# Kernel optimization log

Measured on AMD Instinct MI355X. Metric: run time of the kernel, lower is better.

## Reference

```python
import jax, jax.numpy as jnp
import numpy as np

GRID_SIZE = 4
SPLINE_ORDER = 3
EDGE_DIM = 384


def make_grid():
    # efficient-KAN default grid_range [-1, 1]
    h = 2.0 / GRID_SIZE
    return (jnp.arange(-SPLINE_ORDER, GRID_SIZE + SPLINE_ORDER + 1, dtype=jnp.float32) * h - 1.0)


def b_splines(x, grid, k):
    # x: (N, d); grid: (G+2k+1,) shared across features -> (N, d, G+k)
    xe = x[..., None]
    bases = ((xe >= grid[:-1]) & (xe < grid[1:])).astype(x.dtype)
    for j in range(1, k + 1):
        bases = ((xe - grid[: -(j + 1)]) / (grid[j:-1] - grid[: -(j + 1)]) * bases[..., :-1]
                 + (grid[j + 1:] - xe) / (grid[j + 1:] - grid[1:-j]) * bases[..., 1:])
    return bases


def kan_linear(x, base_W, spline_W, grid):
    # efficient-KAN KANLinear: silu base path + spline path
    base = jax.nn.silu(x) @ base_W.T
    B = b_splines(x, grid, SPLINE_ORDER)          # (N, in, G+k)
    spline = jnp.einsum('nic,oic->no', B, spline_W)
    return base + spline


def gckan_layer(x, edge_index, edge_attr, p, grid):
    ea = edge_attr @ p['edge_W'].T + p['edge_b']          # (E, out)
    xt = x @ p['node_W'].T + p['node_b']                  # (N, out)
    row, col = edge_index[0], edge_index[1]
    msg = ea * xt[row]                                    # gather + multiply
    agg = jnp.zeros_like(xt).at[col].add(msg)             # scatter-add
    return kan_linear(agg, p['base_W'], p['spline_W'], grid)


def _layer_params(key, in_feat, out_feat):
    k1, k2, k3, k4 = jax.random.split(key, 4)
    coef = GRID_SIZE + SPLINE_ORDER
    return {
        'node_W': jax.random.normal(k1, (out_feat, in_feat), jnp.float32) / np.sqrt(in_feat),
        'node_b': jnp.zeros((out_feat,), jnp.float32),
        'edge_W': jax.random.normal(k2, (out_feat, EDGE_DIM), jnp.float32) / np.sqrt(EDGE_DIM),
        'edge_b': jnp.zeros((out_feat,), jnp.float32),
        'base_W': jax.random.normal(k3, (out_feat, out_feat), jnp.float32) / np.sqrt(out_feat),
        'spline_W': jax.random.normal(k4, (out_feat, out_feat, coef), jnp.float32) * (0.1 / np.sqrt(out_feat)),
    }


def setup_inputs() -> dict:
    N, E, F, H, C = 50000, 500000, 256, 256, 32
    key = jax.random.key(0)
    ks = jax.random.split(key, 6)
    inp = {
        'x': jax.random.normal(ks[0], (N, F), jnp.float32),
        'edge_index': jax.random.randint(ks[1], (2, E), 0, N, jnp.int32),
        'edge_attr': jax.random.normal(ks[2], (E, EDGE_DIM), jnp.float32),
    }
    p0 = _layer_params(ks[3], F, H)
    p1 = _layer_params(ks[4], H, H)
    po = _layer_params(ks[5], F + 2 * H, C)
    for tag, p in (('0', p0), ('1', p1), ('o', po)):
        for n, v in p.items():
            inp[n + tag] = v
    return inp


def reference(x, edge_index, edge_attr,
              node_W0, node_b0, edge_W0, edge_b0, base_W0, spline_W0,
              node_W1, node_b1, edge_W1, edge_b1, base_W1, spline_W1,
              node_Wo, node_bo, edge_Wo, edge_bo, base_Wo, spline_Wo):
    grid = make_grid()
    p0 = dict(node_W=node_W0, node_b=node_b0, edge_W=edge_W0, edge_b=edge_b0, base_W=base_W0, spline_W=spline_W0)
    p1 = dict(node_W=node_W1, node_b=node_b1, edge_W=edge_W1, edge_b=edge_b1, base_W=base_W1, spline_W=spline_W1)
    po = dict(node_W=node_Wo, node_b=node_bo, edge_W=edge_Wo, edge_b=edge_bo, base_W=base_Wo, spline_W=spline_Wo)
    skips = [x]
    h = gckan_layer(x, edge_index, edge_attr, p0, grid)
    skips.append(h)
    h = gckan_layer(h, edge_index, edge_attr, p1, grid)
    skips.append(h)
    h = jnp.concatenate(skips, axis=1)  # skip=True concat -> (N, F+2H)
    return gckan_layer(h, edge_index, edge_attr, po, grid)
```

## Files before the change

kernel.cpp:

```cpp
#include <hip/hip_runtime.h>


typedef __attribute__((ext_vector_type(4))) float f32x4;
typedef __attribute__((ext_vector_type(8))) short bf16x8;
typedef __attribute__((ext_vector_type(8))) unsigned short u16x8;
typedef __attribute__((ext_vector_type(4))) unsigned short u16x4;

__device__ __forceinline__ unsigned short f2bf(float f) {
    union { float f; unsigned u; } v; v.f = f;
    unsigned r = v.u + 0x7FFFu + ((v.u >> 16) & 1u);
    return (unsigned short)(r >> 16);
}

__device__ __forceinline__ float bf2f(unsigned short u) {
    union { unsigned u; float f; } v; v.u = ((unsigned)u) << 16;
    return v.f;
}

__device__ __forceinline__ float siluf(float x) {
    return x / (1.0f + __expf(-x));
}

__device__ __forceinline__ void gl16(const void* g, void* l) {
    __builtin_amdgcn_global_load_lds(
        (const __attribute__((address_space(1))) unsigned*)g,
        (__attribute__((address_space(3))) unsigned*)l, 16, 0, 0);
}

__device__ __forceinline__ void expand8(float x, float* o8) {
    float b[10];
#pragma unroll
    for (int i = 0; i < 10; ++i) {
        float ti = 0.5f * i - 2.5f;
        b[i] = (x >= ti && x < ti + 0.5f) ? 1.0f : 0.0f;
    }
#pragma unroll
    for (int j = 1; j <= 3; ++j) {
        float inv = 2.0f / (float)j;
#pragma unroll
        for (int i = 0; i < 10 - j; ++i) {
            float ti = 0.5f * i - 2.5f;
            float tj = 0.5f * (i + j + 1) - 2.5f;
            b[i] = (x - ti) * inv * b[i] + (tj - x) * inv * b[i + 1];
        }
    }
    o8[0] = siluf(x);
#pragma unroll
    for (int c = 0; c < 7; ++c) o8[c + 1] = b[c];
}

__global__ __launch_bounds__(256) void k_hist(
    const int* __restrict__ col, int* __restrict__ cnt, int E) {
    int i = blockIdx.x * 256 + threadIdx.x;
    if (i < E) atomicAdd(&cnt[col[i]], 1);
}

__global__ __launch_bounds__(1024) void k_scan(int* __restrict__ c, int N) {
    __shared__ int wsum[16];
    __shared__ int ctot;
    const int t = threadIdx.x;
    const int lane = t & 63, wid = t >> 6;
    int carry = 0;
    for (int base = 0; base < N; base += 1024) {
        int i = base + t;
        int v0 = (i < N) ? c[i] : 0;
        int v = v0;
#pragma unroll
        for (int off = 1; off < 64; off <<= 1) {
            int n = __shfl_up(v, (unsigned)off, 64);
            if (lane >= off) v += n;
        }
        if (lane == 63) wsum[wid] = v;
        __syncthreads();
        if (t < 16) {
            int s = wsum[t], sv = s;
#pragma unroll
            for (int off = 1; off < 16; off <<= 1) {
                int n = __shfl_up(sv, (unsigned)off, 16);
                if (t >= off) sv += n;
            }
            wsum[t] = sv - s;
            if (t == 15) ctot = sv;
        }
        __syncthreads();
        if (i < N) c[i] = carry + wsum[wid] + v - v0;
        carry += ctot;
        __syncthreads();
    }
}

__global__ __launch_bounds__(256) void k_scatter(
    const int* __restrict__ row, const int* __restrict__ col,
    int* __restrict__ cursor, int* __restrict__ rowS,
    int* __restrict__ colS, int* __restrict__ eidS, int E) {
    int i = blockIdx.x * 256 + threadIdx.x;
    if (i < E) {
        int c = col[i];
        int p = atomicAdd(&cursor[c], 1);
        rowS[p] = row[i];
        colS[p] = c;
        eidS[p] = i;
    }
}

__global__ __launch_bounds__(256) void pack_kt(
    const float* __restrict__ src, unsigned short* __restrict__ dst,
    int N, int K) {
    long idx = (long)blockIdx.x * 256 + threadIdx.x;
    if (idx >= (long)N * K) return;
    int n = (int)(idx / K), k = (int)(idx - (long)n * K);
    long o = (((long)(k >> 5) * 4 + ((k >> 3) & 3)) * N + n) * 8 + (k & 7);
    dst[o] = f2bf(src[idx]);
}

__global__ __launch_bounds__(256) void pack_kan_kt(
    const float* __restrict__ baseW, const float* __restrict__ splineW,
    unsigned short* __restrict__ dst, int N) {
    long idx = (long)blockIdx.x * 256 + threadIdx.x;
    if (idx >= (long)N * 2048) return;
    int n = (int)(idx >> 11), k = (int)(idx & 2047);
    int ic = k >> 3, c = k & 7;
    float v = (c == 0) ? baseW[(long)n * 256 + ic]
                       : splineW[((long)n * 256 + ic) * 7 + (c - 1)];
    long o = (((long)(k >> 5) * 4 + ((k >> 3) & 3)) * N + n) * 8 + (k & 7);
    dst[o] = f2bf(v);
}

template <bool TWO, bool WITH_O>
__global__ __launch_bounds__(256, 1) void ea_gemm4(
    const float* __restrict__ EA,
    const unsigned short* __restrict__ Wp0, const float* __restrict__ b0,
    const unsigned short* __restrict__ Wp1, const float* __restrict__ b1,
    const unsigned short* __restrict__ Wpo, const float* __restrict__ bo,
    unsigned short* __restrict__ O0, unsigned short* __restrict__ O1,
    unsigned short* __restrict__ Oo, int E) {
    constexpr int WOOFF = TWO ? 73728 : 40960;
    constexpr int SMEMSZ = WOOFF + (WITH_O ? 24576 : 0);
    __shared__ __align__(16) char smem[SMEMSZ];

    const int tid = threadIdx.x;
    const int wv = tid >> 6, lane = tid & 63;
    const int l15 = lane & 15, l4 = lane >> 4;
    const long m0 = (long)blockIdx.x * 64;

    f32x4 acc0[4][4] = {};
    f32x4 acc1[4][4] = {};
    f32x4 acco[4] = {};

    const int sr = tid >> 2, sg = tid & 3;
    const long arow = m0 + sr;
    const bool aok = arow < E;
    const float* aptr = EA + arow * 384 + sg * 8;
    const int awoff = sg * 1024 + ((sr ^ (sg << 2))) * 16;

    const char* wp0 = (const char*)Wp0;
    const char* wp1 = (const char*)Wp1;
    const int ci = lane * 16;

    if (WITH_O) {
#pragma unroll
        for (int i = 0; i < 6; ++i) {
            int o = (tid + i * 256) * 16;
            if (o < 24576)
                *(u16x8*)(smem + WOOFF + o) =
                    *(const u16x8*)((const char*)Wpo + o);
        }
    }

#define ISSUE_B(IT, BUF)                                                       \
    {                                                                          \
        _Pragma("unroll")                                                      \
        for (int g = 0; g < 4; ++g) {                                          \
            int ch = g * 4 + wv;                                               \
            gl16(wp0 + (long)(IT) * 16384 + ch * 1024 + ci,                    \
                 smem + 8192 + (BUF) * 16384 + ch * 1024);                     \
        }                                                                      \
        if (TWO) {                                                             \
            _Pragma("unroll")                                                  \
            for (int g = 0; g < 4; ++g) {                                      \
                int ch = g * 4 + wv;                                           \
                gl16(wp1 + (long)(IT) * 16384 + ch * 1024 + ci,                \
                     smem + 40960 + (BUF) * 16384 + ch * 1024);                \
            }                                                                  \
        }                                                                      \
        __builtin_amdgcn_sched_barrier(0);                                     \
    }

#define WRITE_A(BUF)                                                           \
    {                                                                          \
        u16x8 rr = {};                                                         \
        if (aok) {                                                             \
            rr[0] = f2bf(a0v.x); rr[1] = f2bf(a0v.y);                          \
            rr[2] = f2bf(a0v.z); rr[3] = f2bf(a0v.w);                          \
            rr[4] = f2bf(a1v.x); rr[5] = f2bf(a1v.y);                          \
            rr[6] = f2bf(a1v.z); rr[7] = f2bf(a1v.w);                          \
        }                                                                      \
        *(u16x8*)(smem + (BUF) * 4096 + awoff) = rr;                           \
        __builtin_amdgcn_sched_barrier(0);                                     \
    }

    ISSUE_B(0, 0);
    float4 a0v = make_float4(0.f, 0.f, 0.f, 0.f);
    float4 a1v = make_float4(0.f, 0.f, 0.f, 0.f);
    if (aok) { a0v = *(const float4*)(aptr); a1v = *(const float4*)(aptr + 4); }
    WRITE_A(0);
    if (aok) { a0v = *(const float4*)(aptr + 32); a1v = *(const float4*)(aptr + 36); }
    __builtin_amdgcn_sched_barrier(0);

#pragma unroll
    for (int it = 0; it < 12; ++it) {
        if (it == 11) asm volatile("s_waitcnt vmcnt(0)" ::: "memory");
        else          asm volatile("s_waitcnt vmcnt(2)" ::: "memory");
        asm volatile("s_waitcnt lgkmcnt(0)" ::: "memory");
        __builtin_amdgcn_s_barrier();
        __builtin_amdgcn_sched_barrier(0);
        const int buf = it & 1, nbf = buf ^ 1;
        if (it < 11) {
            ISSUE_B(it + 1, nbf);
            WRITE_A(nbf);
            if (it < 10) {
                if (aok) {
                    a0v = *(const float4*)(aptr + (it + 2) * 32);
                    a1v = *(const float4*)(aptr + (it + 2) * 32 + 4);
                }
                __builtin_amdgcn_sched_barrier(0);
            }
        }
        bf16x8 af[4];
#pragma unroll
        for (int mi = 0; mi < 4; ++mi)
            af[mi] = *(const bf16x8*)(smem + buf * 4096 + l4 * 1024 +
                                      (((mi * 16 + l15) ^ (l4 << 2))) * 16);
        {
            bf16x8 bf0[4];
#pragma unroll
            for (int nj = 0; nj < 4; ++nj)
                bf0[nj] = *(const bf16x8*)(smem + 8192 + buf * 16384 + l4 * 4096 +
                                           (wv * 64 + nj * 16 + l15) * 16);
#pragma unroll
            for (int mi = 0; mi < 4; ++mi)
#pragma unroll
                for (int nj = 0; nj < 4; ++nj)
                    acc0[mi][nj] = __builtin_amdgcn_mfma_f32_16x16x32_bf16(
                        af[mi], bf0[nj], acc0[mi][nj], 0, 0, 0);
        }
        if (TWO) {
            bf16x8 bf1[4];
#pragma unroll
            for (int nj = 0; nj < 4; ++nj)
                bf1[nj] = *(const bf16x8*)(smem + 40960 + buf * 16384 + l4 * 4096 +
                                           (wv * 64 + nj * 16 + l15) * 16);
#pragma unroll
            for (int mi = 0; mi < 4; ++mi)
#pragma unroll
                for (int nj = 0; nj < 4; ++nj)
                    acc1[mi][nj] = __builtin_amdgcn_mfma_f32_16x16x32_bf16(
                        af[mi], bf1[nj], acc1[mi][nj], 0, 0, 0);
        }
        if (WITH_O && wv < 2) {
            bf16x8 bov = *(const bf16x8*)(smem + WOOFF + it * 2048 + l4 * 512 +
                                          (wv * 16 + l15) * 16);
#pragma unroll
            for (int mi = 0; mi < 4; ++mi)
                acco[mi] = __builtin_amdgcn_mfma_f32_16x16x32_bf16(
                    af[mi], bov, acco[mi], 0, 0, 0);
        }
    }
#undef ISSUE_B
#undef WRITE_A

    const int nb2 = wv * 64;
    float bs0[4];
#pragma unroll
    for (int nj = 0; nj < 4; ++nj) bs0[nj] = b0[nb2 + nj * 16 + l15];
#pragma unroll
    for (int mi = 0; mi < 4; ++mi) {
#pragma unroll
        for (int r = 0; r < 4; ++r) {
            long e = m0 + mi * 16 + l4 * 4 + r;
            if (e < E) {
                unsigned short* dst = O0 + e * 256 + nb2 + l15;
#pragma unroll
                for (int nj = 0; nj < 4; ++nj)
                    dst[nj * 16] = f2bf(acc0[mi][nj][r] + bs0[nj]);
            }
        }
    }
    if (TWO) {
        float bs1[4];
#pragma unroll
        for (int nj = 0; nj < 4; ++nj) bs1[nj] = b1[nb2 + nj * 16 + l15];
#pragma unroll
        for (int mi = 0; mi < 4; ++mi) {
#pragma unroll
            for (int r = 0; r < 4; ++r) {
                long e = m0 + mi * 16 + l4 * 4 + r;
                if (e < E) {
                    unsigned short* dst = O1 + e * 256 + nb2 + l15;
#pragma unroll
                    for (int nj = 0; nj < 4; ++nj)
                        dst[nj * 16] = f2bf(acc1[mi][nj][r] + bs1[nj]);
                }
            }
        }
    }
    if (WITH_O && wv < 2) {
        float bso = bo[wv * 16 + l15];
#pragma unroll
        for (int mi = 0; mi < 4; ++mi) {
#pragma unroll
            for (int r = 0; r < 4; ++r) {
                long e = m0 + mi * 16 + l4 * 4 + r;
                if (e < E)
                    Oo[e * 32 + wv * 16 + l15] = f2bf(acco[mi][r] + bso);
            }
        }
    }
}

__global__ __launch_bounds__(256) void kan_mfma256_p(
    const float* __restrict__ AGG, const unsigned short* __restrict__ Wp,
    float* __restrict__ Y, int M) {
    __shared__ __align__(16) char smem[8192 + 2 * 16384];
    const int tid = threadIdx.x;
    const int wv = tid >> 6, lane = tid & 63;
    const int l15 = lane & 15, l4 = lane >> 4;
    const long m0 = (long)blockIdx.x * 64;
    f32x4 acc[4][4] = {};

    const int srow = tid & 63, sg = tid >> 6;
    const long arow = m0 + srow;
    const bool aok = arow < M;
    const float* aptr = AGG + arow * 256 + sg;
    const char* wp = (const char*)Wp;
    const int ci = lane * 16;
    const int awoff = sg * 1024 + srow * 16;

#define ISSUE_KB(IT, BUF)                                                      \
    {                                                                          \
        _Pragma("unroll")                                                      \
        for (int g = 0; g < 4; ++g) {                                          \
            int ch = g * 4 + wv;                                               \
            gl16(wp + (long)(IT) * 16384 + ch * 1024 + ci,                     \
                 smem + 8192 + (BUF) * 16384 + ch * 1024);                     \
        }                                                                      \
        __builtin_amdgcn_sched_barrier(0);                                     \
    }

    float xv0 = aok ? aptr[0] : 0.f;
    ISSUE_KB(0, 0);
    {
        float e8[8];
        expand8(xv0, e8);
        u16x8 ap;
#pragma unroll
        for (int c = 0; c < 8; ++c) ap[c] = f2bf(e8[c]);
        *(u16x8*)(smem + awoff) = ap;
    }
    float xv1 = aok ? aptr[4] : 0.f;
    __builtin_amdgcn_sched_barrier(0);

    for (int it = 0; it < 64; ++it) {
        if (it == 63) asm volatile("s_waitcnt vmcnt(0)" ::: "memory");
        else          asm volatile("s_waitcnt vmcnt(1)" ::: "memory");
        asm volatile("s_waitcnt lgkmcnt(0)" ::: "memory");
        __builtin_amdgcn_s_barrier();
        __builtin_amdgcn_sched_barrier(0);
        const int buf = it & 1, nbf = buf ^ 1;
        if (it < 63) {
            ISSUE_KB(it + 1, nbf);
            {
                float e8[8];
                expand8(xv1, e8);
                u16x8 ap;
#pragma unroll
                for (int c = 0; c < 8; ++c) ap[c] = f2bf(e8[c]);
                *(u16x8*)(smem + nbf * 4096 + awoff) = ap;
            }
            __builtin_amdgcn_sched_barrier(0);
            if (it < 62) {
                xv1 = aok ? aptr[(it + 2) * 4] : 0.f;
                __builtin_amdgcn_sched_barrier(0);
            }
        }
        bf16x8 af[4], bfv[4];
#pragma unroll
        for (int mi = 0; mi < 4; ++mi)
            af[mi] = *(const bf16x8*)(smem + buf * 4096 + l4 * 1024 +
                                      (mi * 16 + l15) * 16);
#pragma unroll
        for (int nj = 0; nj < 4; ++nj)
            bfv[nj] = *(const bf16x8*)(smem + 8192 + buf * 16384 + l4 * 4096 +
                                       (wv * 64 + nj * 16 + l15) * 16);
#pragma unroll
        for (int mi = 0; mi < 4; ++mi)
#pragma unroll
            for (int nj = 0; nj < 4; ++nj)
                acc[mi][nj] = __builtin_amdgcn_mfma_f32_16x16x32_bf16(
                    af[mi], bfv[nj], acc[mi][nj], 0, 0, 0);
    }
#undef ISSUE_KB

    const int nb = wv * 64;
#pragma unroll
    for (int mi = 0; mi < 4; ++mi) {
#pragma unroll
        for (int r = 0; r < 4; ++r) {
            long gm = m0 + mi * 16 + l4 * 4 + r;
            if (gm < M) {
#pragma unroll
                for (int nj = 0; nj < 4; ++nj)
                    Y[gm * 256 + nb + nj * 16 + l15] = acc[mi][nj][r];
            }
        }
    }
}

template <int K>
__global__ __launch_bounds__(256) void node_mfma_p(
    const float* __restrict__ X, const unsigned short* __restrict__ Wp,
    const float* __restrict__ bias, unsigned short* __restrict__ Y, int M) {
    __shared__ __align__(16) char smem[8192 + 2 * 16384];
    const int tid = threadIdx.x;
    const int wv = tid >> 6, lane = tid & 63;
    const int l15 = lane & 15, l4 = lane >> 4;
    const long m0 = (long)blockIdx.x * 64;
    f32x4 acc[4][4] = {};
    constexpr int NIT = K / 32;

    const int sr = tid >> 2, sg = tid & 3;
    const long arow = m0 + sr;
    const bool aok = arow < M;
    const float* aptr = X + arow * K + sg * 8;
    const int awoff = sg * 1024 + ((sr ^ (sg << 2))) * 16;
    const char* wp = (const char*)Wp;
    const int ci = lane * 16;

#define ISSUE_NB(IT, BUF)                                                      \
    {                                                                          \
        _Pragma("unroll")                                                      \
        for (int g = 0; g < 4; ++g) {                                          \
            int ch = g * 4 + wv;                                               \
            gl16(wp + (long)(IT) * 16384 + ch * 1024 + ci,                     \
                 smem + 8192 + (BUF) * 16384 + ch * 1024);                     \
        }                                                                      \
        __builtin_amdgcn_sched_barrier(0);                                     \
    }

#define WRITE_NA(BUF)                                                          \
    {                                                                          \
        u16x8 rr = {};                                                         \
        if (aok) {                                                             \
            rr[0] = f2bf(a0v.x); rr[1] = f2bf(a0v.y);                          \
            rr[2] = f2bf(a0v.z); rr[3] = f2bf(a0v.w);                          \
            rr[4] = f2bf(a1v.x); rr[5] = f2bf(a1v.y);                          \
            rr[6] = f2bf(a1v.z); rr[7] = f2bf(a1v.w);                          \
        }                                                                      \
        *(u16x8*)(smem + (BUF) * 4096 + awoff) = rr;                           \
        __builtin_amdgcn_sched_barrier(0);                                     \
    }

    ISSUE_NB(0, 0);
    float4 a0v = make_float4(0.f, 0.f, 0.f, 0.f);
    float4 a1v = make_float4(0.f, 0.f, 0.f, 0.f);
    if (aok) { a0v = *(const float4*)(aptr); a1v = *(const float4*)(aptr + 4); }
    WRITE_NA(0);
    if (aok) { a0v = *(const float4*)(aptr + 32); a1v = *(const float4*)(aptr + 36); }
    __builtin_amdgcn_sched_barrier(0);

#pragma unroll
    for (int it = 0; it < NIT; ++it) {
        if (it == NIT - 1) asm volatile("s_waitcnt vmcnt(0)" ::: "memory");
        else               asm volatile("s_waitcnt vmcnt(2)" ::: "memory");
        asm volatile("s_waitcnt lgkmcnt(0)" ::: "memory");
        __builtin_amdgcn_s_barrier();
        __builtin_amdgcn_sched_barrier(0);
        const int buf = it & 1, nbf = buf ^ 1;
        if (it < NIT - 1) {
            ISSUE_NB(it + 1, nbf);
            WRITE_NA(nbf);
            if (it < NIT - 2) {
                if (aok) {
                    a0v = *(const float4*)(aptr + (it + 2) * 32);
                    a1v = *(const float4*)(aptr + (it + 2) * 32 + 4);
                }
                __builtin_amdgcn_sched_barrier(0);
            }
        }
        bf16x8 af[4], bfv[4];
#pragma unroll
        for (int mi = 0; mi < 4; ++mi)
            af[mi] = *(const bf16x8*)(smem + buf * 4096 + l4 * 1024 +
                                      (((mi * 16 + l15) ^ (l4 << 2))) * 16);
#pragma unroll
        for (int nj = 0; nj < 4; ++nj)
            bfv[nj] = *(const bf16x8*)(smem + 8192 + buf * 16384 + l4 * 4096 +
                                       (wv * 64 + nj * 16 + l15) * 16);
#pragma unroll
        for (int mi = 0; mi < 4; ++mi)
#pragma unroll
            for (int nj = 0; nj < 4; ++nj)
                acc[mi][nj] = __builtin_amdgcn_mfma_f32_16x16x32_bf16(
                    af[mi], bfv[nj], acc[mi][nj], 0, 0, 0);
    }
#undef ISSUE_NB
#undef WRITE_NA

    const int nb = wv * 64;
    float bs[4];
#pragma unroll
    for (int nj = 0; nj < 4; ++nj) bs[nj] = bias[nb + nj * 16 + l15];
#pragma unroll
    for (int mi = 0; mi < 4; ++mi) {
#pragma unroll
        for (int r = 0; r < 4; ++r) {
            long gm = m0 + mi * 16 + l4 * 4 + r;
            if (gm < M) {
#pragma unroll
                for (int nj = 0; nj < 4; ++nj)
                    Y[gm * 256 + nb + nj * 16 + l15] = f2bf(acc[mi][nj][r] + bs[nj]);
            }
        }
    }
}

__global__ __launch_bounds__(256) void msg256(
    const unsigned short* __restrict__ EAr, const unsigned short* __restrict__ XT,
    const int* __restrict__ rowS, const int* __restrict__ colS,
    const int* __restrict__ eidS, float* __restrict__ AGG, int E) {
    __shared__ __align__(16) unsigned short eas[64][264];
    __shared__ int rows_s[64];
    __shared__ int cols_s[64];
    const int tid = threadIdx.x;
    const long m0 = (long)blockIdx.x * 64;

    const int r = tid >> 2, s = tid & 3;
    {
        long p = m0 + r;
        if (p < E) {
            const unsigned short* src = EAr + (long)eidS[p] * 256 + s * 8;
#pragma unroll
            for (int k = 0; k < 8; ++k)
                *(u16x8*)&eas[r][s * 8 + k * 32] = *(const u16x8*)(src + k * 32);
        } else {
            u16x8 z = {};
#pragma unroll
            for (int k = 0; k < 8; ++k) *(u16x8*)&eas[r][s * 8 + k * 32] = z;
        }
    }
    if (tid < 64) {
        long p = m0 + tid;
        cols_s[tid] = (p < E) ? colS[p] : -1;
        rows_s[tid] = (p < E) ? rowS[p] : 0;
    }
    __syncthreads();

    const int c = tid;
    float sum = 0.f;
    int cur = cols_s[0];
    int runstart = 0;
#pragma unroll 1
    for (int g = 0; g < 8; ++g) {
        float xv[8];
#pragma unroll
        for (int j = 0; j < 8; ++j)
            xv[j] = bf2f(XT[(long)rows_s[g * 8 + j] * 256 + c]);
#pragma unroll
        for (int j = 0; j < 8; ++j) {
            int e = g * 8 + j;
            int cc = cols_s[e];
            if (cc != cur) {
                if (cur >= 0) {
                    float* dst = AGG + (long)cur * 256 + c;
                    if (runstart > 0) *dst = sum;
                    else atomicAdd(dst, sum);
                }
                cur = cc; runstart = e; sum = 0.f;
            }
            sum += bf2f(eas[e][c]) * xv[j];
        }
    }
    if (cur >= 0) {
        atomicAdd(AGG + (long)cur * 256 + c, sum);
    }
}

__global__ __launch_bounds__(256) void msg32(
    const unsigned short* __restrict__ EAro, const unsigned short* __restrict__ XT,
    const int* __restrict__ rowS, const int* __restrict__ colS,
    const int* __restrict__ eidS, float* __restrict__ AGG, int E) {
    __shared__ __align__(16) unsigned short eas[256][36];
    __shared__ int rows_s[256];
    __shared__ int cols_s[256];
    __shared__ int eid_s[256];
    const int tid = threadIdx.x;
    const long m0 = (long)blockIdx.x * 256;

    {
        long p = m0 + tid;
        cols_s[tid] = (p < E) ? colS[p] : -1;
        rows_s[tid] = (p < E) ? rowS[p] : 0;
        eid_s[tid]  = (p < E) ? eidS[p] : -1;
    }
    __syncthreads();
    const int rr0 = tid >> 2, s = tid & 3;
#pragma unroll
    for (int ps = 0; ps < 4; ++ps) {
        int rr = ps * 64 + rr0;
        int eid = eid_s[rr];
        u16x8 v = {};
        if (eid >= 0) v = *(const u16x8*)(EAro + (long)eid * 32 + s * 8);
        *(u16x8*)&eas[rr][s * 8] = v;
    }
    __syncthreads();

    const int c = tid & 31, sb = tid >> 5;
    const int e0 = sb * 32;
    float sum = 0.f;
    int cur = cols_s[e0];
    int runstart = e0;
#pragma unroll 1
    for (int g = 0; g < 4; ++g) {
        float xv[8];
#pragma unroll
        for (int j = 0; j < 8; ++j)
            xv[j] = bf2f(XT[(long)rows_s[e0 + g * 8 + j] * 32 + c]);
#pragma unroll
        for (int j = 0; j < 8; ++j) {
            int e = e0 + g * 8 + j;
            int cc = cols_s[e];
            if (cc != cur) {
                if (cur >= 0) {
                    float* dst = AGG + (long)cur * 32 + c;
                    if (runstart > 0 && cols_s[runstart - 1] != cur) *dst = sum;
                    else atomicAdd(dst, sum);
                }
                cur = cc; runstart = e; sum = 0.f;
            }
            sum += bf2f(eas[e][c]) * xv[j];
        }
    }
    if (cur >= 0) {
        int eend = e0 + 32;
        float* dst = AGG + (long)cur * 32 + c;
        bool oks = (runstart > 0 && cols_s[runstart - 1] != cur);
        bool oke = (eend < 256 && cols_s[eend] != cur);
        if (oks && oke) *dst = sum;
        else atomicAdd(dst, sum);
    }
}

__global__ __launch_bounds__(256) void node_cat_mfma(
    const float* __restrict__ X, const float* __restrict__ H0,
    const float* __restrict__ H1, const unsigned short* __restrict__ Wh,
    const float* __restrict__ bias, unsigned short* __restrict__ Y, int M) {
    __shared__ __align__(16) unsigned short As[4][256][8];
    __shared__ __align__(16) unsigned short Bs[4][32][8];
    const int tid = threadIdx.x;
    const int wv = tid >> 6, lane = tid & 63;
    const int l15 = lane & 15, l4 = lane >> 4;
    const long m0 = (long)blockIdx.x * 256;
    f32x4 acc[4][2] = {};

    const int sr = tid >> 3;
    const int sq = (tid & 7) * 4;
    const int sg2 = sq >> 3, so2 = sq & 7;

    for (int it = 0; it < 24; ++it) {
        const int k0 = it * 32;
        const float* src = (it < 8) ? X : (it < 16) ? H0 : H1;
        const int kk = k0 & 255;
        float4 va[8];
#pragma unroll
        for (int j = 0; j < 8; ++j) {
            long r_ = m0 + j * 32 + sr;
            va[j] = (r_ < M) ? *(const float4*)(src + r_ * 256 + kk + sq)
                             : make_float4(0.f, 0.f, 0.f, 0.f);
        }
        u16x8 bv = {};
        if (tid < 128)
            bv = *(const u16x8*)(Wh + (long)(tid >> 2) * 768 + k0 + (tid & 3) * 8);
        __syncthreads();
#pragma unroll
        for (int j = 0; j < 8; ++j) {
            u16x4 ap;
            ap[0] = f2bf(va[j].x); ap[1] = f2bf(va[j].y);
            ap[2] = f2bf(va[j].z); ap[3] = f2bf(va[j].w);
            *(u16x4*)&As[sg2][j * 32 + sr][so2] = ap;
        }
        if (tid < 128) *(u16x8*)&Bs[tid & 3][tid >> 2][0] = bv;
        __syncthreads();
        bf16x8 af[4], bfv[2];
#pragma unroll
        for (int mi = 0; mi < 4; ++mi)
            af[mi] = *(const bf16x8*)&As[l4][wv * 64 + mi * 16 + l15][0];
#pragma unroll
        for (int nj = 0; nj < 2; ++nj)
            bfv[nj] = *(const bf16x8*)&Bs[l4][nj * 16 + l15][0];
#pragma unroll
        for (int mi = 0; mi < 4; ++mi)
#pragma unroll
            for (int nj = 0; nj < 2; ++nj)
                acc[mi][nj] = __builtin_amdgcn_mfma_f32_16x16x32_bf16(
                    af[mi], bfv[nj], acc[mi][nj], 0, 0, 0);
    }

#pragma unroll
    for (int mi = 0; mi < 4; ++mi) {
#pragma unroll
        for (int r = 0; r < 4; ++r) {
            long gm = m0 + wv * 64 + mi * 16 + l4 * 4 + r;
            if (gm < M) {
#pragma unroll
                for (int nj = 0; nj < 2; ++nj) {
                    int o = nj * 16 + l15;
                    Y[gm * 32 + o] = f2bf(acc[mi][nj][r] + bias[o]);
                }
            }
        }
    }
}

__global__ __launch_bounds__(256) void kan_gemm32(
    const float* __restrict__ AGG, const float* __restrict__ Wc,
    float* __restrict__ Y, int M) {
    __shared__ float As[64][36];
    __shared__ float Bs[32][36];
    const int tid = threadIdx.x;
    const int tx = tid & 15, ty = tid >> 4;
    const int m0 = blockIdx.x * 64;
    float acc[4][2] = {{0.f, 0.f}, {0.f, 0.f}, {0.f, 0.f}, {0.f, 0.f}};
    const int er = tid >> 2, ef = tid & 3;
    const int em = m0 + er;
    for (int ic = 0; ic < 32; ic += 4) {
        float xv = (em < M) ? AGG[(long)em * 32 + ic + ef] : 0.f;
        float e8[8];
        expand8(xv, e8);
        *(float4*)&As[er][ef * 8] = make_float4(e8[0], e8[1], e8[2], e8[3]);
        *(float4*)&As[er][ef * 8 + 4] = make_float4(e8[4], e8[5], e8[6], e8[7]);
        {
            int o = tid >> 3, k4 = (tid & 7) * 4;
            *(float4*)&Bs[o][k4] = *(const float4*)&Wc[(long)o * 256 + ic * 8 + k4];
        }
        __syncthreads();
#pragma unroll
        for (int kk = 0; kk < 32; ++kk) {
            float a_[4], b_[2];
#pragma unroll
            for (int i = 0; i < 4; ++i) a_[i] = As[ty * 4 + i][kk];
#pragma unroll
            for (int j = 0; j < 2; ++j) b_[j] = Bs[tx * 2 + j][kk];
#pragma unroll
            for (int i = 0; i < 4; ++i)
#pragma unroll
                for (int j = 0; j < 2; ++j) acc[i][j] = fmaf(a_[i], b_[j], acc[i][j]);
        }
        __syncthreads();
    }
#pragma unroll
    for (int i = 0; i < 4; ++i) {
        int gm = m0 + ty * 4 + i;
        if (gm >= M) continue;
#pragma unroll
        for (int j = 0; j < 2; ++j) Y[(long)gm * 32 + tx * 2 + j] = acc[i][j];
    }
}

__global__ __launch_bounds__(256) void cvt_bf16(
    const float* __restrict__ s, unsigned short* __restrict__ d, int n) {
    int i = blockIdx.x * 256 + threadIdx.x;
    if (i < n) d[i] = f2bf(s[i]);
}

__global__ __launch_bounds__(256) void pack_kan_f32(
    const float* __restrict__ baseW, const float* __restrict__ splineW,
    float* __restrict__ Wc, int n) {
    int idx = blockIdx.x * 256 + threadIdx.x;
    if (idx >= n) return;
    float* dst = Wc + (long)idx * 8;
    dst[0] = baseW[idx];
    const float* sw = splineW + (long)idx * 7;
#pragma unroll
    for (int c = 0; c < 7; ++c) dst[1 + c] = sw[c];
}

extern "C" void kernel_launch(void* const* d_in, const int* in_sizes, int n_in,
                              void* d_out, int out_size, void* d_ws, size_t ws_size,
                              hipStream_t stream) {
    const float* x          = (const float*)d_in[0];
    const int*   edge_index = (const int*)d_in[1];
    const float* edge_attr  = (const float*)d_in[2];
    const float* node_W0 = (const float*)d_in[3];
    const float* node_b0 = (const float*)d_in[4];
    const float* edge_W0 = (const float*)d_in[5];
    const float* edge_b0 = (const float*)d_in[6];
    const float* base_W0 = (const float*)d_in[7];
    const float* spline_W0 = (const float*)d_in[8];
    const float* node_W1 = (const float*)d_in[9];
    const float* node_b1 = (const float*)d_in[10];
    const float* edge_W1 = (const float*)d_in[11];
    const float* edge_b1 = (const float*)d_in[12];
    const float* base_W1 = (const float*)d_in[13];
    const float* spline_W1 = (const float*)d_in[14];
    const float* node_Wo = (const float*)d_in[15];
    const float* node_bo = (const float*)d_in[16];
    const float* edge_Wo = (const float*)d_in[17];
    const float* edge_bo = (const float*)d_in[18];
    const float* base_Wo = (const float*)d_in[19];
    const float* spline_Wo = (const float*)d_in[20];
    float* out = (float*)d_out;

    const int N = in_sizes[0] / 256;
    const int E = in_sizes[1] / 2;

    float* ws  = (float*)d_ws;
    unsigned short* xt = (unsigned short*)ws;
    float* agg = ws + (long)N * 256;
    float* h0  = agg + (long)N * 256;
    float* h1  = h0 + (long)N * 256;
    float* Wco = h1 + (long)N * 256;
    unsigned short* Wp0  = (unsigned short*)(Wco + 32 * 256);
    unsigned short* Wp1  = Wp0 + 98304;
    unsigned short* Wpo  = Wp1 + 98304;
    unsigned short* nWp0 = Wpo + 12288;
    unsigned short* nWp1 = nWp0 + 65536;
    unsigned short* Wc0p = nWp1 + 65536;
    unsigned short* Wc1p = Wc0p + 524288;
    unsigned short* nWoh = Wc1p + 524288;
    int* cursor = (int*)(nWoh + 24576);
    int* rowS   = cursor + (N + 1);
    int* colS   = rowS + E;
    int* eidS   = colS + E;
    unsigned short* EAr0 = (unsigned short*)(((uintptr_t)(eidS + E) + 255) & ~(uintptr_t)255);
    const int nt256 = (E + 255) / 256;
    const long Epad = (long)nt256 * 256;
    unsigned short* EAr1 = EAr0 + Epad * 256;

    const size_t need2 = (size_t)((char*)(EAr1 + Epad * 256 + Epad * 32) - (char*)d_ws);
    const bool two = ws_size >= need2;
    unsigned short* EAro = two ? (EAr1 + Epad * 256) : (EAr0 + Epad * 256);

    const int* row = edge_index;
    const int* col = edge_index + E;

    const int nb64 = (N + 63) / 64;
    const int eb64 = (E + 63) / 64;
    const int eb256 = (E + 255) / 256;
    const int nb256 = (N + 255) / 256;

    hipMemsetAsync(cursor, 0, (size_t)(N + 1) * sizeof(int), stream);
    k_hist<<<eb256, 256, 0, stream>>>(col, cursor, E);
    k_scan<<<1, 1024, 0, stream>>>(cursor, N);
    k_scatter<<<eb256, 256, 0, stream>>>(row, col, cursor, rowS, colS, eidS, E);

    pack_kt<<<(256 * 384 + 255) / 256, 256, 0, stream>>>(edge_W0, Wp0, 256, 384);
    pack_kt<<<(256 * 384 + 255) / 256, 256, 0, stream>>>(edge_W1, Wp1, 256, 384);
    pack_kt<<<(32 * 384 + 255) / 256, 256, 0, stream>>>(edge_Wo, Wpo, 32, 384);
    pack_kt<<<(256 * 256 + 255) / 256, 256, 0, stream>>>(node_W0, nWp0, 256, 256);
    pack_kt<<<(256 * 256 + 255) / 256, 256, 0, stream>>>(node_W1, nWp1, 256, 256);
    pack_kan_kt<<<(256 * 2048 + 255) / 256, 256, 0, stream>>>(base_W0, spline_W0, Wc0p, 256);
    pack_kan_kt<<<(256 * 2048 + 255) / 256, 256, 0, stream>>>(base_W1, spline_W1, Wc1p, 256);
    cvt_bf16<<<(32 * 768 + 255) / 256, 256, 0, stream>>>(node_Wo, nWoh, 32 * 768);
    pack_kan_f32<<<(32 * 32 + 255) / 256, 256, 0, stream>>>(base_Wo, spline_Wo, Wco, 32 * 32);

    if (two) {
        ea_gemm4<true, true><<<eb64, 256, 0, stream>>>(
            edge_attr, Wp0, edge_b0, Wp1, edge_b1, Wpo, edge_bo,
            EAr0, EAr1, EAro, E);
    } else {
        ea_gemm4<false, true><<<eb64, 256, 0, stream>>>(
            edge_attr, Wp0, edge_b0, Wp0, edge_b0, Wpo, edge_bo,
            EAr0, EAr0, EAro, E);
    }

    hipMemsetAsync(agg, 0, (size_t)N * 256 * sizeof(float), stream);
    node_mfma_p<256><<<nb64, 256, 0, stream>>>(x, nWp0, node_b0, xt, N);
    msg256<<<eb64, 256, 0, stream>>>(EAr0, xt, rowS, colS, eidS, agg, E);
    kan_mfma256_p<<<nb64, 256, 0, stream>>>(agg, Wc0p, h0, N);

    if (!two) {
        ea_gemm4<false, false><<<eb64, 256, 0, stream>>>(
            edge_attr, Wp1, edge_b1, Wp1, edge_b1, Wpo, edge_bo,
            EAr0, EAr0, EAro, E);
    }
    hipMemsetAsync(agg, 0, (size_t)N * 256 * sizeof(float), stream);
    node_mfma_p<256><<<nb64, 256, 0, stream>>>(h0, nWp1, node_b1, xt, N);
    msg256<<<eb64, 256, 0, stream>>>(two ? EAr1 : EAr0, xt, rowS, colS, eidS, agg, E);
    kan_mfma256_p<<<nb64, 256, 0, stream>>>(agg, Wc1p, h1, N);

    hipMemsetAsync(agg, 0, (size_t)N * 32 * sizeof(float), stream);
    node_cat_mfma<<<nb256, 256, 0, stream>>>(x, h0, h1, nWoh, node_bo, xt, N);
    msg32<<<eb256, 256, 0, stream>>>(EAro, xt, rowS, colS, eidS, agg, E);
    kan_gemm32<<<nb64, 256, 0, stream>>>(agg, Wco, out, N);
}
```

Before: 1.533 ms.

## Replace LDS-staged edge GEMM with per-wave direct-load MFMA tiles

Rewrites the edge-attribute projection kernel so each wave handles its own 16 edges against all 256 (or 512) output columns. Weights are read straight from global memory and the A fragment is converted in registers, so there is no LDS staging, no double buffering and no block barriers. Launch bounds are raised to allow two blocks per CU. In exchange, weight reuse across waves now depends on L1/L2 instead of shared memory, and the per-lane output stores stay strided.

```diff
diff --git a/kernel.cpp b/kernel.cpp
--- a/kernel.cpp
+++ b/kernel.cpp
@@ -127,192 +127,84 @@
 }
 
 template <bool TWO, bool WITH_O>
-__global__ __launch_bounds__(256, 1) void ea_gemm4(
+__global__ __launch_bounds__(256, 2) void ea_gemm5(
     const float* __restrict__ EA,
     const unsigned short* __restrict__ Wp0, const float* __restrict__ b0,
     const unsigned short* __restrict__ Wp1, const float* __restrict__ b1,
     const unsigned short* __restrict__ Wpo, const float* __restrict__ bo,
     unsigned short* __restrict__ O0, unsigned short* __restrict__ O1,
     unsigned short* __restrict__ Oo, int E) {
-    constexpr int WOOFF = TWO ? 73728 : 40960;
-    constexpr int SMEMSZ = WOOFF + (WITH_O ? 24576 : 0);
-    __shared__ __align__(16) char smem[SMEMSZ];
-
     const int tid = threadIdx.x;
     const int wv = tid >> 6, lane = tid & 63;
     const int l15 = lane & 15, l4 = lane >> 4;
-    const long m0 = (long)blockIdx.x * 64;
-
-    f32x4 acc0[4][4] = {};
-    f32x4 acc1[4][4] = {};
-    f32x4 acco[4] = {};
-
-    const int sr = tid >> 2, sg = tid & 3;
-    const long arow = m0 + sr;
+    const long m0 = (long)blockIdx.x * 64 + wv * 16;
+
+    f32x4 acc0[16] = {};
+    f32x4 acc1[16] = {};
+    f32x4 acco[2] = {};
+
+    const long arow = m0 + l15;
     const bool aok = arow < E;
-    const float* aptr = EA + arow * 384 + sg * 8;
-    const int awoff = sg * 1024 + ((sr ^ (sg << 2))) * 16;
-
-    const char* wp0 = (const char*)Wp0;
-    const char* wp1 = (const char*)Wp1;
-    const int ci = lane * 16;
-
-    if (WITH_O) {
-#pragma unroll
-        for (int i = 0; i < 6; ++i) {
-            int o = (tid + i * 256) * 16;
-            if (o < 24576)
-                *(u16x8*)(smem + WOOFF + o) =
-                    *(const u16x8*)((const char*)Wpo + o);
-        }
-    }
-
-#define ISSUE_B(IT, BUF)                                                       \
-    {                                                                          \
-        _Pragma("unroll")                                                      \
-        for (int g = 0; g < 4; ++g) {                                          \
-            int ch = g * 4 + wv;                                               \
-            gl16(wp0 + (long)(IT) * 16384 + ch * 1024 + ci,                    \
-                 smem + 8192 + (BUF) * 16384 + ch * 1024);                     \
-        }                                                                      \
-        if (TWO) {                                                             \
-            _Pragma("unroll")                                                  \
-            for (int g = 0; g < 4; ++g) {                                      \
-                int ch = g * 4 + wv;                                           \
-                gl16(wp1 + (long)(IT) * 16384 + ch * 1024 + ci,                \
-                     smem + 40960 + (BUF) * 16384 + ch * 1024);                \
-            }                                                                  \
-        }                                                                      \
-        __builtin_amdgcn_sched_barrier(0);                                     \
-    }
-
-#define WRITE_A(BUF)                                                           \
-    {                                                                          \
-        u16x8 rr = {};                                                         \
-        if (aok) {                                                             \
-            rr[0] = f2bf(a0v.x); rr[1] = f2bf(a0v.y);                          \
-            rr[2] = f2bf(a0v.z); rr[3] = f2bf(a0v.w);                          \
-            rr[4] = f2bf(a1v.x); rr[5] = f2bf(a1v.y);                          \
-            rr[6] = f2bf(a1v.z); rr[7] = f2bf(a1v.w);                          \
-        }                                                                      \
-        *(u16x8*)(smem + (BUF) * 4096 + awoff) = rr;                           \
-        __builtin_amdgcn_sched_barrier(0);                                     \
-    }
-
-    ISSUE_B(0, 0);
-    float4 a0v = make_float4(0.f, 0.f, 0.f, 0.f);
-    float4 a1v = make_float4(0.f, 0.f, 0.f, 0.f);
-    if (aok) { a0v = *(const float4*)(aptr); a1v = *(const float4*)(aptr + 4); }
-    WRITE_A(0);
-    if (aok) { a0v = *(const float4*)(aptr + 32); a1v = *(const float4*)(aptr + 36); }
-    __builtin_amdgcn_sched_barrier(0);
-
-#pragma unroll
+    const float* aptr = EA + arow * 384 + l4 * 8;
+    const unsigned short* bp0 = Wp0 + l4 * 2048 + l15 * 8;
+    const unsigned short* bp1 = Wp1 + l4 * 2048 + l15 * 8;
+    const unsigned short* bpo = Wpo + l4 * 256 + l15 * 8;
+
+#pragma unroll 2
     for (int it = 0; it < 12; ++it) {
-        if (it == 11) asm volatile("s_waitcnt vmcnt(0)" ::: "memory");
-        else          asm volatile("s_waitcnt vmcnt(2)" ::: "memory");
-        asm volatile("s_waitcnt lgkmcnt(0)" ::: "memory");
-        __builtin_amdgcn_s_barrier();
-        __builtin_amdgcn_sched_barrier(0);
-        const int buf = it & 1, nbf = buf ^ 1;
-        if (it < 11) {
-            ISSUE_B(it + 1, nbf);
-            WRITE_A(nbf);
-            if (it < 10) {
-                if (aok) {
-                    a0v = *(const float4*)(aptr + (it + 2) * 32);
-                    a1v = *(const float4*)(aptr + (it + 2) * 32 + 4);
-                }
-                __builtin_amdgcn_sched_barrier(0);
-            }
-        }
-        bf16x8 af[4];
-#pragma unroll
-        for (int mi = 0; mi < 4; ++mi)
-            af[mi] = *(const bf16x8*)(smem + buf * 4096 + l4 * 1024 +
-                                      (((mi * 16 + l15) ^ (l4 << 2))) * 16);
-        {
-            bf16x8 bf0[4];
-#pragma unroll
-            for (int nj = 0; nj < 4; ++nj)
-                bf0[nj] = *(const bf16x8*)(smem + 8192 + buf * 16384 + l4 * 4096 +
-                                           (wv * 64 + nj * 16 + l15) * 16);
-#pragma unroll
-            for (int mi = 0; mi < 4; ++mi)
-#pragma unroll
-                for (int nj = 0; nj < 4; ++nj)
-                    acc0[mi][nj] = __builtin_amdgcn_mfma_f32_16x16x32_bf16(
-                        af[mi], bf0[nj], acc0[mi][nj], 0, 0, 0);
-        }
-        if (TWO) {
-            bf16x8 bf1[4];
-#pragma unroll
-            for (int nj = 0; nj < 4; ++nj)
-                bf1[nj] = *(const bf16x8*)(smem + 40960 + buf * 16384 + l4 * 4096 +
-                                           (wv * 64 + nj * 16 + l15) * 16);
-#pragma unroll
-            for (int mi = 0; mi < 4; ++mi)
-#pragma unroll
-                for (int nj = 0; nj < 4; ++nj)
-                    acc1[mi][nj] = __builtin_amdgcn_mfma_f32_16x16x32_bf16(
-                        af[mi], bf1[nj], acc1[mi][nj], 0, 0, 0);
-        }
-        if (WITH_O && wv < 2) {
-            bf16x8 bov = *(const bf16x8*)(smem + WOOFF + it * 2048 + l4 * 512 +
-                                          (wv * 16 + l15) * 16);
-#pragma unroll
-            for (int mi = 0; mi < 4; ++mi)
-                acco[mi] = __builtin_amdgcn_mfma_f32_16x16x32_bf16(
-                    af[mi], bov, acco[mi], 0, 0, 0);
-        }
-    }
-#undef ISSUE_B
-#undef WRITE_A
-
-    const int nb2 = wv * 64;
-    float bs0[4];
-#pragma unroll
-    for (int nj = 0; nj < 4; ++nj) bs0[nj] = b0[nb2 + nj * 16 + l15];
-#pragma unroll
-    for (int mi = 0; mi < 4; ++mi) {
-#pragma unroll
-        for (int r = 0; r < 4; ++r) {
-            long e = m0 + mi * 16 + l4 * 4 + r;
-            if (e < E) {
-                unsigned short* dst = O0 + e * 256 + nb2 + l15;
-#pragma unroll
-                for (int nj = 0; nj < 4; ++nj)
-                    dst[nj * 16] = f2bf(acc0[mi][nj][r] + bs0[nj]);
-            }
-        }
-    }
-    if (TWO) {
-        float bs1[4];
-#pragma unroll
-        for (int nj = 0; nj < 4; ++nj) bs1[nj] = b1[nb2 + nj * 16 + l15];
-#pragma unroll
-        for (int mi = 0; mi < 4; ++mi) {
-#pragma unroll
-            for (int r = 0; r < 4; ++r) {
-                long e = m0 + mi * 16 + l4 * 4 + r;
-                if (e < E) {
-                    unsigned short* dst = O1 + e * 256 + nb2 + l15;
-#pragma unroll
-                    for (int nj = 0; nj < 4; ++nj)
-                        dst[nj * 16] = f2bf(acc1[mi][nj][r] + bs1[nj]);
-                }
-            }
-        }
-    }
-    if (WITH_O && wv < 2) {
-        float bso = bo[wv * 16 + l15];
-#pragma unroll
-        for (int mi = 0; mi < 4; ++mi) {
-#pragma unroll
-            for (int r = 0; r < 4; ++r) {
-                long e = m0 + mi * 16 + l4 * 4 + r;
-                if (e < E)
-                    Oo[e * 32 + wv * 16 + l15] = f2bf(acco[mi][r] + bso);
+        u16x8 au = {};
+        if (aok) {
+            float4 v0 = *(const float4*)(aptr + it * 32);
+            float4 v1 = *(const float4*)(aptr + it * 32 + 4);
+            au[0] = f2bf(v0.x); au[1] = f2bf(v0.y); au[2] = f2bf(v0.z); au[3] = f2bf(v0.w);
+            au[4] = f2bf(v1.x); au[5] = f2bf(v1.y); au[6] = f2bf(v1.z); au[7] = f2bf(v1.w);
+        }
+        bf16x8 af;
+        __builtin_memcpy(&af, &au, sizeof(af));
+
+        const unsigned short* w0 = bp0 + it * 8192;
+        const unsigned short* w1 = bp1 + it * 8192;
+#pragma unroll
+        for (int nj = 0; nj < 16; ++nj) {
+            bf16x8 bf0 = *(const bf16x8*)(w0 + nj * 128);
+            acc0[nj] = __builtin_amdgcn_mfma_f32_16x16x32_bf16(
+                af, bf0, acc0[nj], 0, 0, 0);
+            if (TWO) {
+                bf16x8 bf1 = *(const bf16x8*)(w1 + nj * 128);
+                acc1[nj] = __builtin_amdgcn_mfma_f32_16x16x32_bf16(
+                    af, bf1, acc1[nj], 0, 0, 0);
+            }
+        }
+        if (WITH_O) {
+            const unsigned short* wo = bpo + it * 1024;
+#pragma unroll
+            for (int nj = 0; nj < 2; ++nj) {
+                bf16x8 bfo = *(const bf16x8*)(wo + nj * 128);
+                acco[nj] = __builtin_amdgcn_mfma_f32_16x16x32_bf16(
+                    af, bfo, acco[nj], 0, 0, 0);
+            }
+        }
+    }
+
+#pragma unroll
+    for (int r = 0; r < 4; ++r) {
+        long e = m0 + l4 * 4 + r;
+        if (e < E) {
+            unsigned short* d0 = O0 + e * 256 + l15;
+#pragma unroll
+            for (int nj = 0; nj < 16; ++nj)
+                d0[nj * 16] = f2bf(acc0[nj][r] + b0[nj * 16 + l15]);
+            if (TWO) {
+                unsigned short* d1 = O1 + e * 256 + l15;
+#pragma unroll
+                for (int nj = 0; nj < 16; ++nj)
+                    d1[nj * 16] = f2bf(acc1[nj][r] + b1[nj * 16 + l15]);
+            }
+            if (WITH_O) {
+                unsigned short* dd = Oo + e * 32 + l15;
+#pragma unroll
+                for (int nj = 0; nj < 2; ++nj)
+                    dd[nj * 16] = f2bf(acco[nj][r] + bo[nj * 16 + l15]);
             }
         }
     }
@@ -864,11 +756,11 @@
     pack_kan_f32<<<(32 * 32 + 255) / 256, 256, 0, stream>>>(base_Wo, spline_Wo, Wco, 32 * 32);
 
     if (two) {
-        ea_gemm4<true, true><<<eb64, 256, 0, stream>>>(
+        ea_gemm5<true, true><<<eb64, 256, 0, stream>>>(
             edge_attr, Wp0, edge_b0, Wp1, edge_b1, Wpo, edge_bo,
             EAr0, EAr1, EAro, E);
     } else {
-        ea_gemm4<false, true><<<eb64, 256, 0, stream>>>(
+        ea_gemm5<false, true><<<eb64, 256, 0, stream>>>(
             edge_attr, Wp0, edge_b0, Wp0, edge_b0, Wpo, edge_bo,
             EAr0, EAr0, EAro, E);
     }
@@ -879,7 +771,7 @@
     kan_mfma256_p<<<nb64, 256, 0, stream>>>(agg, Wc0p, h0, N);
 
     if (!two) {
-        ea_gemm4<false, false><<<eb64, 256, 0, stream>>>(
+        ea_gemm5<false, false><<<eb64, 256, 0, stream>>>(
             edge_attr, Wp1, edge_b1, Wp1, edge_b1, Wpo, edge_bo,
             EAr0, EAr0, EAro, E);
     }
```

Result: slower. 1.761 ms (+14.9%).

## Triple-buffer weight tiles and prefetch edge_attr two steps ahead in edge GEMM

Applied to the files above, without the earlier changes.

The edge-attribute GEMM moves its B-weight shared-memory staging from double to triple buffering. Weight tiles are issued two K-steps ahead, and edge_attr rows are loaded into two alternating register sets so global loads run further ahead of the MFMA work. The vmcnt waits are retuned to match the deeper queue of outstanding loads. The cost is more LDS (about 106KB with both layers) and more live registers, and the hand-counted waitcnt values are fragile if the number of issued loads changes.

```diff
diff --git a/kernel.cpp b/kernel.cpp
--- a/kernel.cpp
+++ b/kernel.cpp
@@ -127,14 +127,15 @@
 }
 
 template <bool TWO, bool WITH_O>
-__global__ __launch_bounds__(256, 1) void ea_gemm4(
+__global__ __launch_bounds__(256, 1) void ea_gemm6(
     const float* __restrict__ EA,
     const unsigned short* __restrict__ Wp0, const float* __restrict__ b0,
     const unsigned short* __restrict__ Wp1, const float* __restrict__ b1,
     const unsigned short* __restrict__ Wpo, const float* __restrict__ bo,
     unsigned short* __restrict__ O0, unsigned short* __restrict__ O1,
     unsigned short* __restrict__ Oo, int E) {
-    constexpr int WOOFF = TWO ? 73728 : 40960;
+    constexpr int BSZ = TWO ? 32768 : 16384;
+    constexpr int WOOFF = 8192 + 3 * BSZ;
     constexpr int SMEMSZ = WOOFF + (WITH_O ? 24576 : 0);
     __shared__ __align__(16) char smem[SMEMSZ];
 
@@ -161,81 +162,102 @@
 #pragma unroll
         for (int i = 0; i < 6; ++i) {
             int o = (tid + i * 256) * 16;
-            if (o < 24576)
-                *(u16x8*)(smem + WOOFF + o) =
-                    *(const u16x8*)((const char*)Wpo + o);
-        }
-    }
-
-#define ISSUE_B(IT, BUF)                                                       \
+            *(u16x8*)(smem + WOOFF + o) = *(const u16x8*)((const char*)Wpo + o);
+        }
+    }
+
+#define ISSUE_B6(IT, BUF)                                                      \
     {                                                                          \
         _Pragma("unroll")                                                      \
         for (int g = 0; g < 4; ++g) {                                          \
             int ch = g * 4 + wv;                                               \
             gl16(wp0 + (long)(IT) * 16384 + ch * 1024 + ci,                    \
-                 smem + 8192 + (BUF) * 16384 + ch * 1024);                     \
+                 smem + 8192 + (BUF) * BSZ + ch * 1024);                       \
         }                                                                      \
         if (TWO) {                                                             \
             _Pragma("unroll")                                                  \
             for (int g = 0; g < 4; ++g) {                                      \
                 int ch = g * 4 + wv;                                           \
                 gl16(wp1 + (long)(IT) * 16384 + ch * 1024 + ci,                \
-                     smem + 40960 + (BUF) * 16384 + ch * 1024);                \
+                     smem + 8192 + (BUF) * BSZ + 16384 + ch * 1024);           \
             }                                                                  \
         }                                                                      \
         __builtin_amdgcn_sched_barrier(0);                                     \
     }
 
-#define WRITE_A(BUF)                                                           \
+#define WRITE_A6(IT, VA, VB)                                                   \
     {                                                                          \
         u16x8 rr = {};                                                         \
         if (aok) {                                                             \
-            rr[0] = f2bf(a0v.x); rr[1] = f2bf(a0v.y);                          \
-            rr[2] = f2bf(a0v.z); rr[3] = f2bf(a0v.w);                          \
-            rr[4] = f2bf(a1v.x); rr[5] = f2bf(a1v.y);                          \
-            rr[6] = f2bf(a1v.z); rr[7] = f2bf(a1v.w);                          \
+            rr[0] = f2bf((VA).x); rr[1] = f2bf((VA).y);                        \
+            rr[2] = f2bf((VA).z); rr[3] = f2bf((VA).w);                        \
+            rr[4] = f2bf((VB).x); rr[5] = f2bf((VB).y);                        \
+            rr[6] = f2bf((VB).z); rr[7] = f2bf((VB).w);                        \
         }                                                                      \
-        *(u16x8*)(smem + (BUF) * 4096 + awoff) = rr;                           \
+        *(u16x8*)(smem + ((IT) & 1) * 4096 + awoff) = rr;                      \
         __builtin_amdgcn_sched_barrier(0);                                     \
     }
 
-    ISSUE_B(0, 0);
-    float4 a0v = make_float4(0.f, 0.f, 0.f, 0.f);
-    float4 a1v = make_float4(0.f, 0.f, 0.f, 0.f);
-    if (aok) { a0v = *(const float4*)(aptr); a1v = *(const float4*)(aptr + 4); }
-    WRITE_A(0);
-    if (aok) { a0v = *(const float4*)(aptr + 32); a1v = *(const float4*)(aptr + 36); }
+    const float4 z4 = make_float4(0.f, 0.f, 0.f, 0.f);
+    {
+        float4 s0 = z4, s1 = z4;
+        if (aok) { s0 = *(const float4*)(aptr); s1 = *(const float4*)(aptr + 4); }
+        WRITE_A6(0, s0, s1);
+    }
+    float4 r1a = z4, r1b = z4, r0a = z4, r0b = z4;
+    if (aok) { r1a = *(const float4*)(aptr + 32); r1b = *(const float4*)(aptr + 36); }
     __builtin_amdgcn_sched_barrier(0);
+    ISSUE_B6(0, 0);
+    if (aok) { r0a = *(const float4*)(aptr + 64); r0b = *(const float4*)(aptr + 68); }
+    __builtin_amdgcn_sched_barrier(0);
+    ISSUE_B6(1, 1);
 
 #pragma unroll
     for (int it = 0; it < 12; ++it) {
-        if (it == 11) asm volatile("s_waitcnt vmcnt(0)" ::: "memory");
-        else          asm volatile("s_waitcnt vmcnt(2)" ::: "memory");
+        if (it <= 9) {
+            if (TWO) asm volatile("s_waitcnt vmcnt(10)" ::: "memory");
+            else     asm volatile("s_waitcnt vmcnt(6)"  ::: "memory");
+        } else if (it == 10) {
+            if (TWO) asm volatile("s_waitcnt vmcnt(8)" ::: "memory");
+            else     asm volatile("s_waitcnt vmcnt(4)" ::: "memory");
+        } else {
+            asm volatile("s_waitcnt vmcnt(0)" ::: "memory");
+        }
         asm volatile("s_waitcnt lgkmcnt(0)" ::: "memory");
         __builtin_amdgcn_s_barrier();
         __builtin_amdgcn_sched_barrier(0);
-        const int buf = it & 1, nbf = buf ^ 1;
+
         if (it < 11) {
-            ISSUE_B(it + 1, nbf);
-            WRITE_A(nbf);
-            if (it < 10) {
+            if ((it + 1) & 1) { WRITE_A6(it + 1, r1a, r1b); }
+            else              { WRITE_A6(it + 1, r0a, r0b); }
+        }
+        if (it <= 8) {
+            if ((it + 3) & 1) {
                 if (aok) {
-                    a0v = *(const float4*)(aptr + (it + 2) * 32);
-                    a1v = *(const float4*)(aptr + (it + 2) * 32 + 4);
+                    r1a = *(const float4*)(aptr + (it + 3) * 32);
+                    r1b = *(const float4*)(aptr + (it + 3) * 32 + 4);
                 }
-                __builtin_amdgcn_sched_barrier(0);
-            }
-        }
+            } else {
+                if (aok) {
+                    r0a = *(const float4*)(aptr + (it + 3) * 32);
+                    r0b = *(const float4*)(aptr + (it + 3) * 32 + 4);
+                }
+            }
+            __builtin_amdgcn_sched_barrier(0);
+        }
+        if (it <= 9) { ISSUE_B6(it + 2, (it + 2) % 3); }
+
+        const int abuf = it & 1, bbuf = it % 3;
         bf16x8 af[4];
 #pragma unroll
         for (int mi = 0; mi < 4; ++mi)
-            af[mi] = *(const bf16x8*)(smem + buf * 4096 + l4 * 1024 +
+            af[mi] = *(const bf16x8*)(smem + abuf * 4096 + l4 * 1024 +
                                       (((mi * 16 + l15) ^ (l4 << 2))) * 16);
         {
             bf16x8 bf0[4];
 #pragma unroll
             for (int nj = 0; nj < 4; ++nj)
-                bf0[nj] = *(const bf16x8*)(smem + 8192 + buf * 16384 + l4 * 4096 +
+                bf0[nj] = *(const bf16x8*)(smem + 8192 + bbuf * BSZ + l4 * 4096 +
                                            (wv * 64 + nj * 16 + l15) * 16);
 #pragma unroll
             for (int mi = 0; mi < 4; ++mi)
@@ -248,8 +270,8 @@
             bf16x8 bf1[4];
 #pragma unroll
             for (int nj = 0; nj < 4; ++nj)
-                bf1[nj] = *(const bf16x8*)(smem + 40960 + buf * 16384 + l4 * 4096 +
-                                           (wv * 64 + nj * 16 + l15) * 16);
+                bf1[nj] = *(const bf16x8*)(smem + 8192 + bbuf * BSZ + 16384 +
+                                           l4 * 4096 + (wv * 64 + nj * 16 + l15) * 16);
 #pragma unroll
             for (int mi = 0; mi < 4; ++mi)
 #pragma unroll
@@ -266,8 +288,8 @@
                     af[mi], bov, acco[mi], 0, 0, 0);
         }
     }
-#undef ISSUE_B
-#undef WRITE_A
+#undef ISSUE_B6
+#undef WRITE_A6
 
     const int nb2 = wv * 64;
     float bs0[4];
@@ -864,11 +886,11 @@
     pack_kan_f32<<<(32 * 32 + 255) / 256, 256, 0, stream>>>(base_Wo, spline_Wo, Wco, 32 * 32);
 
     if (two) {
-        ea_gemm4<true, true><<<eb64, 256, 0, stream>>>(
+        ea_gemm6<true, true><<<eb64, 256, 0, stream>>>(
             edge_attr, Wp0, edge_b0, Wp1, edge_b1, Wpo, edge_bo,
             EAr0, EAr1, EAro, E);
     } else {
-        ea_gemm4<false, true><<<eb64, 256, 0, stream>>>(
+        ea_gemm6<false, true><<<eb64, 256, 0, stream>>>(
             edge_attr, Wp0, edge_b0, Wp0, edge_b0, Wpo, edge_bo,
             EAr0, EAr0, EAro, E);
     }
@@ -879,7 +901,7 @@
     kan_mfma256_p<<<nb64, 256, 0, stream>>>(agg, Wc0p, h0, N);
 
     if (!two) {
-        ea_gemm4<false, false><<<eb64, 256, 0, stream>>>(
+        ea_gemm6<false, false><<<eb64, 256, 0, stream>>>(
             edge_attr, Wp1, edge_b1, Wp1, edge_b1, Wpo, edge_bo,
             EAr0, EAr0, EAro, E);
     }
```

Result: faster. 1.459 ms (-4.8%).
